# Optimization experiments

Measured on AMD Instinct MI355X. Metric: run time of the kernel, lower is better.

## Reference

```python
import jax, jax.numpy as jnp
import numpy as np

EMB = 512
HEADS = 8
KEY_DIM = 64


def setup_inputs() -> dict:
    key = jax.random.key(0)
    k1, k2, k3, k4, k5 = jax.random.split(key, 5)
    B, S = 4, 2048
    x = jax.random.normal(k1, (B, S, EMB), dtype=jnp.float32)
    keys = jax.random.normal(k2, (B, HEADS, S, KEY_DIM), dtype=jnp.float32)
    values = jax.random.normal(k3, (B, HEADS, S, KEY_DIM), dtype=jnp.float32)
    # torch.rand -> uniform [0,1)
    query_weights = jax.random.uniform(k4, (EMB, KEY_DIM * HEADS), dtype=jnp.float32)
    output_weights = jax.random.uniform(k5, (KEY_DIM * HEADS, EMB), dtype=jnp.float32)
    return {"x": x, "keys": keys, "values": values,
            "query_weights": query_weights, "output_weights": output_weights}


def reference(x, keys, values, query_weights, output_weights):
    B, S, _ = x.shape
    # Q projection: [B,S,E] @ [E,H*K] -> [B,H,S,K]
    q = (x @ query_weights).reshape(B, S, HEADS, KEY_DIM).transpose(0, 2, 1, 3)
    # scores: [B,H,S,S]
    scores = jnp.einsum('bhqk,bhsk->bhqs', q, keys) / jnp.sqrt(jnp.float32(KEY_DIM))
    attn = jax.nn.softmax(scores, axis=-1)
    # context: [B,H,S,K] -> [B,S,H*K]
    ctx = jnp.einsum('bhqs,bhsk->bhqk', attn, values)
    ctx = ctx.transpose(0, 2, 1, 3).reshape(B, S, HEADS * KEY_DIM)
    return ctx @ output_weights
```

## Files before the change

kernel.cpp:

```cpp
#include <hip/hip_runtime.h>
#include <hip/hip_bf16.h>

#define EMB 512
#define HEADS 8
#define KD 64
#define SEQ 2048
#define BATCH 4

typedef __attribute__((ext_vector_type(8))) short bf16x8;
typedef __attribute__((ext_vector_type(4))) float f32x4;

__device__ __forceinline__ unsigned short f2bf(float x) {
    union { float f; unsigned u; } v; v.f = x;
    unsigned r = v.u + 0x7fff + ((v.u >> 16) & 1);
    return (unsigned short)(r >> 16);
}
__device__ __forceinline__ float bf2f(unsigned short b) {
    union { unsigned u; float f; } v; v.u = ((unsigned)b) << 16;
    return v.f;
}

__global__ __launch_bounds__(256) void prep_k_kernel(const float* __restrict__ K,
                                                     unsigned short* __restrict__ kimg) {
    const int bt = blockIdx.x;
    const float4* src = (const float4*)(K + (size_t)bt * 4096);
    unsigned short* dhi = kimg + (size_t)bt * 8192;
    unsigned short* dlo = dhi + 4096;
#pragma unroll
    for (int it = 0; it < 4; ++it) {
        const int idx = threadIdx.x + it * 256;
        const float4 v = src[idx];
        const unsigned short h0 = f2bf(v.x), h1 = f2bf(v.y),
                             h2 = f2bf(v.z), h3 = f2bf(v.w);
        *(uint2*)&dhi[idx * 4] = make_uint2(
            (unsigned)h0 | ((unsigned)h1 << 16),
            (unsigned)h2 | ((unsigned)h3 << 16));
        *(uint2*)&dlo[idx * 4] = make_uint2(
            (unsigned)f2bf(v.x - bf2f(h0)) | ((unsigned)f2bf(v.y - bf2f(h1)) << 16),
            (unsigned)f2bf(v.z - bf2f(h2)) | ((unsigned)f2bf(v.w - bf2f(h3)) << 16));
    }
}

__global__ __launch_bounds__(256) void prep_v_kernel(const float* __restrict__ V,
                                                     unsigned short* __restrict__ vimg) {
    const int bt = blockIdx.x;
    const float* src = V + (size_t)bt * 4096;
    unsigned short* dst = vimg + (size_t)bt * 4096;
#pragma unroll
    for (int it = 0; it < 2; ++it) {
        const int idx = threadIdx.x + it * 256;
        const int sp  = idx & 31;
        const int d4  = (idx >> 5) << 2;
        const float4 a = *(const float4*)(src + (2 * sp) * KD + d4);
        const float4 b = *(const float4*)(src + (2 * sp + 1) * KD + d4);
#pragma unroll
        for (int j = 0; j < 4; ++j) {
            const float aj = (&a.x)[j], bj = (&b.x)[j];
            *(unsigned*)&dst[(d4 + j) * 64 + 2 * sp] =
                (unsigned)f2bf(aj) | ((unsigned)f2bf(bj) << 16);
        }
    }
}

template <int PREP>
__global__ __launch_bounds__(256) void attn3_kernel(const float* __restrict__ Q,
                                                    const float* __restrict__ Keys,
                                                    const float* __restrict__ Vals,
                                                    const unsigned short* __restrict__ kimg,
                                                    const unsigned short* __restrict__ vimg,
                                                    float* __restrict__ out) {
    constexpr int NT  = 64;
    constexpr int LDK = 72;

    __shared__ unsigned short k_s[2][NT][LDK];
    __shared__ unsigned short v_t[KD][LDK];
    __shared__ unsigned short p_s[4][16][LDK];

    const int t  = threadIdx.x;
    const int w  = t >> 6;
    const int l  = t & 63;
    const int g  = l >> 4;
    const int ln = l & 15;

    const int bh = blockIdx.y;
    const int q0 = blockIdx.x * 64 + w * 16;

    const float* kbase = Keys + (size_t)bh * SEQ * KD;
    const float* vbase = Vals + (size_t)bh * SEQ * KD;
    const float* qptr  = Q + ((size_t)bh * SEQ + q0 + ln) * KD;

    bf16x8 qhi[2], qlo[2];
#pragma unroll
    for (int kk = 0; kk < 2; ++kk) {
        const float* p = qptr + g * 8 + 32 * kk;
#pragma unroll
        for (int j = 0; j < 8; ++j) {
            const float x = p[j] * 0.125f;
            const unsigned short h = f2bf(x);
            qhi[kk][j] = (short)h;
            qlo[kk][j] = (short)f2bf(x - bf2f(h));
        }
    }

    f32x4 acc[4];
#pragma unroll
    for (int db = 0; db < 4; ++db) acc[db] = (f32x4){0.f, 0.f, 0.f, 0.f};
    float m_run = -1e30f, l_run = 0.0f;

    for (int tile = 0; tile < SEQ / NT; ++tile) {
        __syncthreads();

        if (PREP) {
            const uint4* ksrc = (const uint4*)(kimg + (size_t)(bh * 32 + tile) * 8192);
#pragma unroll
            for (int it = 0; it < 4; ++it) {
                const int idx = t + it * 256;
                const int hl  = idx >> 9;
                const int rem = idx & 511;
                *(uint4*)&k_s[hl][rem >> 3][(rem & 7) * 8] = ksrc[idx];
            }
            const uint4* vsrc = (const uint4*)(vimg + (size_t)(bh * 32 + tile) * 4096);
#pragma unroll
            for (int it = 0; it < 2; ++it) {
                const int idx = t + it * 256;
                *(uint4*)&v_t[idx >> 3][(idx & 7) * 8] = vsrc[idx];
            }
        } else {
            const float* kt = kbase + (size_t)tile * NT * KD;
            const float* vt = vbase + (size_t)tile * NT * KD;
#pragma unroll
            for (int it = 0; it < 4; ++it) {
                const int idx = t + it * 256;
                const int s   = idx >> 4;
                const int d4  = (idx & 15) << 2;
                const float4 kv = *(const float4*)(kt + s * KD + d4);
                unsigned short h0 = f2bf(kv.x), h1 = f2bf(kv.y),
                               h2 = f2bf(kv.z), h3 = f2bf(kv.w);
                *(uint2*)&k_s[0][s][d4] = make_uint2(
                    (unsigned)h0 | ((unsigned)h1 << 16),
                    (unsigned)h2 | ((unsigned)h3 << 16));
                *(uint2*)&k_s[1][s][d4] = make_uint2(
                    (unsigned)f2bf(kv.x - bf2f(h0)) | ((unsigned)f2bf(kv.y - bf2f(h1)) << 16),
                    (unsigned)f2bf(kv.z - bf2f(h2)) | ((unsigned)f2bf(kv.w - bf2f(h3)) << 16));
            }
#pragma unroll
            for (int it = 0; it < 2; ++it) {
                const int idx = t + it * 256;
                const int sp  = idx & 31;
                const int d4  = (idx >> 5) << 2;
                const float* v0 = vt + (2 * sp) * KD + d4;
                const float4 a = *(const float4*)v0;
                const float4 b = *(const float4*)(v0 + KD);
#pragma unroll
                for (int j = 0; j < 4; ++j) {
                    const float aj = (&a.x)[j], bj = (&b.x)[j];
                    *(unsigned*)&v_t[d4 + j][2 * sp] =
                        (unsigned)f2bf(aj) | ((unsigned)f2bf(bj) << 16);
                }
            }
        }
        __syncthreads();

        f32x4 st[4];
#pragma unroll
        for (int sb = 0; sb < 4; ++sb) {
            f32x4 c = (f32x4){0.f, 0.f, 0.f, 0.f};
#pragma unroll
            for (int kk = 0; kk < 2; ++kk) {
                const bf16x8 khi = *(const bf16x8*)&k_s[0][sb * 16 + ln][g * 8 + 32 * kk];
                const bf16x8 klo = *(const bf16x8*)&k_s[1][sb * 16 + ln][g * 8 + 32 * kk];
                c = __builtin_amdgcn_mfma_f32_16x16x32_bf16(klo, qhi[kk], c, 0, 0, 0);
                c = __builtin_amdgcn_mfma_f32_16x16x32_bf16(khi, qlo[kk], c, 0, 0, 0);
                c = __builtin_amdgcn_mfma_f32_16x16x32_bf16(khi, qhi[kk], c, 0, 0, 0);
            }
            st[sb] = c;
        }

        float tm = st[0][0];
#pragma unroll
        for (int sb = 0; sb < 4; ++sb)
#pragma unroll
            for (int r = 0; r < 4; ++r) tm = fmaxf(tm, st[sb][r]);
        tm = fmaxf(tm, __shfl_xor(tm, 16));
        tm = fmaxf(tm, __shfl_xor(tm, 32));

        const float m_new  = fmaxf(m_run, tm);
        const float scalef = __expf(m_run - m_new);
        m_run = m_new;

        float rs = 0.f;
#pragma unroll
        for (int sb = 0; sb < 4; ++sb) {
            const float p0 = __expf(st[sb][0] - m_new);
            const float p1 = __expf(st[sb][1] - m_new);
            const float p2 = __expf(st[sb][2] - m_new);
            const float p3 = __expf(st[sb][3] - m_new);
            rs += (p0 + p1) + (p2 + p3);
            const unsigned lo = (unsigned)f2bf(p0) | ((unsigned)f2bf(p1) << 16);
            const unsigned hi = (unsigned)f2bf(p2) | ((unsigned)f2bf(p3) << 16);
            *(uint2*)&p_s[w][ln][sb * 16 + g * 4] = make_uint2(lo, hi);
        }
        rs += __shfl_xor(rs, 16);
        rs += __shfl_xor(rs, 32);
        l_run = l_run * scalef + rs;

#pragma unroll
        for (int r = 0; r < 4; ++r) {
            const float sr = __shfl(scalef, 4 * g + r);
#pragma unroll
            for (int db = 0; db < 4; ++db) acc[db][r] *= sr;
        }

        bf16x8 pa[2];
#pragma unroll
        for (int kk = 0; kk < 2; ++kk)
            pa[kk] = *(const bf16x8*)&p_s[w][ln][g * 8 + 32 * kk];
#pragma unroll
        for (int db = 0; db < 4; ++db) {
            f32x4 c = acc[db];
#pragma unroll
            for (int kk = 0; kk < 2; ++kk) {
                const bf16x8 vb = *(const bf16x8*)&v_t[ln + 16 * db][g * 8 + 32 * kk];
                c = __builtin_amdgcn_mfma_f32_16x16x32_bf16(pa[kk], vb, c, 0, 0, 0);
            }
            acc[db] = c;
        }
    }

    const float invl = 1.0f / l_run;
    const int b = bh >> 3, h = bh & 7;
#pragma unroll
    for (int r = 0; r < 4; ++r) {
        const float iv = __shfl(invl, 4 * g + r);
        float* orow = out + ((size_t)(b * SEQ + q0 + 4 * g + r) * EMB) + h * KD + ln;
#pragma unroll
        for (int db = 0; db < 4; ++db) orow[16 * db] = acc[db][r] * iv;
    }
}

template <int TRANSQ>
__global__ __launch_bounds__(256) void proj_mfma_kernel(const float* __restrict__ in,
                                                        const float* __restrict__ W,
                                                        float* __restrict__ out) {
    __shared__ unsigned short x_s[2][64][72];
    __shared__ unsigned short w_t[2][64][72];

    const int t  = threadIdx.x;
    const int w  = t >> 6;
    const int l  = t & 63;
    const int g  = l >> 4;
    const int ln = l & 15;

    const int row0 = blockIdx.x * 64;
    const int n0   = blockIdx.y * 64;

    f32x4 acc[4];
#pragma unroll
    for (int cb = 0; cb < 4; ++cb) acc[cb] = (f32x4){0.f, 0.f, 0.f, 0.f};

    for (int ch = 0; ch < EMB / 64; ++ch) {
        __syncthreads();
#pragma unroll
        for (int it = 0; it < 4; ++it) {
            const int idx = t + it * 256;
            const int s   = idx >> 4;
            const int d4  = (idx & 15) << 2;
            const float4 xv = *(const float4*)(in + (size_t)(row0 + s) * EMB + ch * 64 + d4);
            const unsigned short h0 = f2bf(xv.x), h1 = f2bf(xv.y),
                                 h2 = f2bf(xv.z), h3 = f2bf(xv.w);
            *(uint2*)&x_s[0][s][d4] = make_uint2(
                (unsigned)h0 | ((unsigned)h1 << 16),
                (unsigned)h2 | ((unsigned)h3 << 16));
            *(uint2*)&x_s[1][s][d4] = make_uint2(
                (unsigned)f2bf(xv.x - bf2f(h0)) | ((unsigned)f2bf(xv.y - bf2f(h1)) << 16),
                (unsigned)f2bf(xv.z - bf2f(h2)) | ((unsigned)f2bf(xv.w - bf2f(h3)) << 16));
        }
#pragma unroll
        for (int it = 0; it < 2; ++it) {
            const int idx = t + it * 256;
            const int sp  = idx & 31;
            const int c4  = (idx >> 5) << 2;
            const float* wrow = W + (size_t)(ch * 64 + 2 * sp) * EMB + n0 + c4;
            const float4 a = *(const float4*)wrow;
            const float4 b = *(const float4*)(wrow + EMB);
#pragma unroll
            for (int j = 0; j < 4; ++j) {
                const float aj = (&a.x)[j], bj = (&b.x)[j];
                const unsigned short ah = f2bf(aj), bh = f2bf(bj);
                *(unsigned*)&w_t[0][c4 + j][2 * sp] =
                    (unsigned)ah | ((unsigned)bh << 16);
                *(unsigned*)&w_t[1][c4 + j][2 * sp] =
                    (unsigned)f2bf(aj - bf2f(ah)) | ((unsigned)f2bf(bj - bf2f(bh)) << 16);
            }
        }
        __syncthreads();

        bf16x8 ah[2], al[2];
#pragma unroll
        for (int kk = 0; kk < 2; ++kk) {
            ah[kk] = *(const bf16x8*)&x_s[0][w * 16 + ln][g * 8 + 32 * kk];
            al[kk] = *(const bf16x8*)&x_s[1][w * 16 + ln][g * 8 + 32 * kk];
        }
#pragma unroll
        for (int cb = 0; cb < 4; ++cb) {
            f32x4 c = acc[cb];
#pragma unroll
            for (int kk = 0; kk < 2; ++kk) {
                const bf16x8 bh = *(const bf16x8*)&w_t[0][cb * 16 + ln][g * 8 + 32 * kk];
                const bf16x8 bl = *(const bf16x8*)&w_t[1][cb * 16 + ln][g * 8 + 32 * kk];
                c = __builtin_amdgcn_mfma_f32_16x16x32_bf16(al[kk], bh, c, 0, 0, 0);
                c = __builtin_amdgcn_mfma_f32_16x16x32_bf16(ah[kk], bl, c, 0, 0, 0);
                c = __builtin_amdgcn_mfma_f32_16x16x32_bf16(ah[kk], bh, c, 0, 0, 0);
            }
            acc[cb] = c;
        }
    }

#pragma unroll
    for (int cb = 0; cb < 4; ++cb) {
#pragma unroll
        for (int r = 0; r < 4; ++r) {
            const int row = row0 + w * 16 + 4 * g + r;
            const int col = n0 + cb * 16 + ln;
            if (TRANSQ) {
                const int b = row >> 11, s = row & 2047;
                const int h = col >> 6, k = col & 63;
                out[((size_t)(b * HEADS + h) * SEQ + s) * KD + k] = acc[cb][r];
            } else {
                out[(size_t)row * EMB + col] = acc[cb][r];
            }
        }
    }
}

__global__ __launch_bounds__(256) void proj_fp32_kernel(const float* __restrict__ in,
                                                        const float* __restrict__ W,
                                                        float* __restrict__ out) {
    __shared__ float x_s[8][EMB];
    const int block_row = blockIdx.x * 8;

    const float4* in4 = (const float4*)(in + (size_t)block_row * EMB);
    float4* xs4 = (float4*)(&x_s[0][0]);
    for (int i = threadIdx.x; i < 8 * EMB / 4; i += 256) xs4[i] = in4[i];
    __syncthreads();

    const int n  = (threadIdx.x & 127) * 4;
    const int rg = threadIdx.x >> 7;

    float acc[4][4] = {};
    for (int e = 0; e < EMB; ++e) {
        const float4 w4 = *(const float4*)(W + (size_t)e * EMB + n);
#pragma unroll
        for (int rr = 0; rr < 4; ++rr) {
            const float xv = x_s[rg + rr * 2][e];
            acc[rr][0] += xv * w4.x;
            acc[rr][1] += xv * w4.y;
            acc[rr][2] += xv * w4.z;
            acc[rr][3] += xv * w4.w;
        }
    }
#pragma unroll
    for (int rr = 0; rr < 4; ++rr) {
        const int row = block_row + rg + rr * 2;
        float4 o;
        o.x = acc[rr][0]; o.y = acc[rr][1]; o.z = acc[rr][2]; o.w = acc[rr][3];
        *(float4*)(out + (size_t)row * EMB + n) = o;
    }
}

extern "C" void kernel_launch(void* const* d_in, const int* in_sizes, int n_in,
                              void* d_out, int out_size, void* d_ws, size_t ws_size,
                              hipStream_t stream) {
    const float* x  = (const float*)d_in[0];
    const float* ks = (const float*)d_in[1];
    const float* vs = (const float*)d_in[2];
    const float* wq = (const float*)d_in[3];
    const float* wo = (const float*)d_in[4];
    float* out = (float*)d_out;

    const size_t QBYTES  = (size_t)BATCH * HEADS * SEQ * KD * 4;
    const size_t CBYTES  = (size_t)BATCH * SEQ * EMB * 4;
    const size_t KIBYTES = (size_t)BATCH * HEADS * SEQ * KD * 2 * 2;
    const size_t VIBYTES = (size_t)BATCH * HEADS * SEQ * KD * 2;

    float* Q = (float*)d_ws;
    const bool mid_ws  = ws_size >= QBYTES + CBYTES;
    const bool full_ws = ws_size >= QBYTES + CBYTES + KIBYTES + VIBYTES;
    float* ctx = mid_ws ? (float*)((char*)d_ws + QBYTES) : out;
    unsigned short* kimg = (unsigned short*)((char*)d_ws + QBYTES + CBYTES);
    unsigned short* vimg = (unsigned short*)((char*)d_ws + QBYTES + CBYTES + KIBYTES);

    const int M = BATCH * SEQ;

    proj_mfma_kernel<1><<<dim3(M / 64, EMB / 64), dim3(256), 0, stream>>>(x, wq, Q);

    if (full_ws) {
        prep_k_kernel<<<dim3(BATCH * HEADS * 32), dim3(256), 0, stream>>>(ks, kimg);
        prep_v_kernel<<<dim3(BATCH * HEADS * 32), dim3(256), 0, stream>>>(vs, vimg);
        attn3_kernel<1><<<dim3(SEQ / 64, BATCH * HEADS), dim3(256), 0, stream>>>(
            Q, ks, vs, kimg, vimg, ctx);
    } else {
        attn3_kernel<0><<<dim3(SEQ / 64, BATCH * HEADS), dim3(256), 0, stream>>>(
            Q, ks, vs, nullptr, nullptr, ctx);
    }

    if (mid_ws) {
        proj_mfma_kernel<0><<<dim3(M / 64, EMB / 64), dim3(256), 0, stream>>>(ctx, wo, out);
    } else {
        proj_fp32_kernel<<<dim3(M / 8), dim3(256), 0, stream>>>(ctx, wo, out);
    }
}
```

Measured before the change: 282.3 us.

## Pre-convert all operands to bf16 tile images and chain bf16 kernels

```diff
diff --git a/kernel.cpp b/kernel.cpp
--- a/kernel.cpp
+++ b/kernel.cpp
@@ -18,6 +18,371 @@
 __device__ __forceinline__ float bf2f(unsigned short b) {
     union { unsigned u; float f; } v; v.u = ((unsigned)b) << 16;
     return v.f;
+}
+__device__ __forceinline__ unsigned pk2(float a, float b) {
+    __hip_bfloat162 h = __float22bfloat162_rn(float2{a, b});
+    unsigned u; __builtin_memcpy(&u, &h, 4); return u;
+}
+
+__global__ __launch_bounds__(256) void prep_all_kernel(
+    const float* __restrict__ x,  const float* __restrict__ wq,
+    const float* __restrict__ wo, const float* __restrict__ K,
+    const float* __restrict__ V,
+    unsigned short* __restrict__ ximg, unsigned short* __restrict__ wqimg,
+    unsigned short* __restrict__ woimg, unsigned short* __restrict__ kimg,
+    unsigned short* __restrict__ vimg) {
+    const int bid = blockIdx.x;
+    const int t   = threadIdx.x;
+
+    if (bid < 1024) {
+        const int rb = bid >> 3, ch = bid & 7;
+        const float* src = x + (size_t)rb * 64 * EMB + ch * 64;
+        unsigned short* dhi = ximg + (size_t)bid * 8192;
+        unsigned short* dlo = dhi + 4096;
+#pragma unroll
+        for (int it = 0; it < 4; ++it) {
+            const int idx = t + it * 256;
+            const int row = idx >> 4, c4 = (idx & 15) << 2;
+            const float4 v = *(const float4*)(src + (size_t)row * EMB + c4);
+            const unsigned short h0 = f2bf(v.x), h1 = f2bf(v.y),
+                                 h2 = f2bf(v.z), h3 = f2bf(v.w);
+            *(uint2*)&dhi[row * 64 + c4] = make_uint2(
+                (unsigned)h0 | ((unsigned)h1 << 16),
+                (unsigned)h2 | ((unsigned)h3 << 16));
+            *(uint2*)&dlo[row * 64 + c4] = make_uint2(
+                (unsigned)f2bf(v.x - bf2f(h0)) | ((unsigned)f2bf(v.y - bf2f(h1)) << 16),
+                (unsigned)f2bf(v.z - bf2f(h2)) | ((unsigned)f2bf(v.w - bf2f(h3)) << 16));
+        }
+    } else if (bid < 1152) {
+        int widx = bid - 1024;
+        const bool isq = widx < 64;
+        if (!isq) widx -= 64;
+        const int nb = widx >> 3, ch = widx & 7;
+        const float* src = (isq ? wq : wo) + (size_t)(ch * 64) * EMB + nb * 64;
+        unsigned short* dhi = isq ? (wqimg + (size_t)widx * 8192)
+                                  : (woimg + (size_t)widx * 4096);
+        unsigned short* dlo = dhi + 4096;
+#pragma unroll
+        for (int it = 0; it < 2; ++it) {
+            const int idx = t + it * 256;
+            const int sp  = idx & 31;
+            const int c4  = (idx >> 5) << 2;
+            const float* r0 = src + (size_t)(2 * sp) * EMB + c4;
+            const float4 a = *(const float4*)r0;
+            const float4 b = *(const float4*)(r0 + EMB);
+#pragma unroll
+            for (int j = 0; j < 4; ++j) {
+                const float aj = (&a.x)[j], bj = (&b.x)[j];
+                const unsigned short ah = f2bf(aj), bh = f2bf(bj);
+                *(unsigned*)&dhi[(c4 + j) * 64 + 2 * sp] =
+                    (unsigned)ah | ((unsigned)bh << 16);
+                if (isq)
+                    *(unsigned*)&dlo[(c4 + j) * 64 + 2 * sp] =
+                        (unsigned)f2bf(aj - bf2f(ah)) | ((unsigned)f2bf(bj - bf2f(bh)) << 16);
+            }
+        }
+    } else if (bid < 2176) {
+        const int kt = bid - 1152;
+        const float4* src = (const float4*)(K + (size_t)kt * 4096);
+        unsigned short* dhi = kimg + (size_t)kt * 8192;
+        unsigned short* dlo = dhi + 4096;
+#pragma unroll
+        for (int it = 0; it < 4; ++it) {
+            const int idx = t + it * 256;
+            const float4 v = src[idx];
+            const unsigned short h0 = f2bf(v.x), h1 = f2bf(v.y),
+                                 h2 = f2bf(v.z), h3 = f2bf(v.w);
+            *(uint2*)&dhi[idx * 4] = make_uint2(
+                (unsigned)h0 | ((unsigned)h1 << 16),
+                (unsigned)h2 | ((unsigned)h3 << 16));
+            *(uint2*)&dlo[idx * 4] = make_uint2(
+                (unsigned)f2bf(v.x - bf2f(h0)) | ((unsigned)f2bf(v.y - bf2f(h1)) << 16),
+                (unsigned)f2bf(v.z - bf2f(h2)) | ((unsigned)f2bf(v.w - bf2f(h3)) << 16));
+        }
+    } else {
+        const int vt = bid - 2176;
+        const float* src = V + (size_t)vt * 4096;
+        unsigned short* dst = vimg + (size_t)vt * 4096;
+#pragma unroll
+        for (int it = 0; it < 2; ++it) {
+            const int idx = t + it * 256;
+            const int sp  = idx & 31;
+            const int d4  = (idx >> 5) << 2;
+            const float4 a = *(const float4*)(src + (2 * sp) * KD + d4);
+            const float4 b = *(const float4*)(src + (2 * sp + 1) * KD + d4);
+#pragma unroll
+            for (int j = 0; j < 4; ++j) {
+                *(unsigned*)&dst[(d4 + j) * 64 + 2 * sp] =
+                    (unsigned)f2bf((&a.x)[j]) | ((unsigned)f2bf((&b.x)[j]) << 16);
+            }
+        }
+    }
+}
+
+__global__ __launch_bounds__(256) void proj_q_kernel(
+    const unsigned short* __restrict__ ximg,
+    const unsigned short* __restrict__ wqimg,
+    unsigned short* __restrict__ qhi_img,
+    unsigned short* __restrict__ qlo_img) {
+    __shared__ unsigned short x_s[2][64][72];
+    __shared__ unsigned short w_t[2][64][72];
+
+    const int t  = threadIdx.x;
+    const int w  = t >> 6;
+    const int l  = t & 63;
+    const int g  = l >> 4;
+    const int ln = l & 15;
+
+    const int rb = blockIdx.x;
+    const int nb = blockIdx.y;
+
+    f32x4 acc[4];
+#pragma unroll
+    for (int cb = 0; cb < 4; ++cb) acc[cb] = (f32x4){0.f, 0.f, 0.f, 0.f};
+
+    for (int ch = 0; ch < 8; ++ch) {
+        __syncthreads();
+        const uint4* xs = (const uint4*)(ximg + (size_t)(rb * 8 + ch) * 8192);
+        const uint4* ws = (const uint4*)(wqimg + (size_t)(nb * 8 + ch) * 8192);
+#pragma unroll
+        for (int it = 0; it < 4; ++it) {
+            const int idx = t + it * 256;
+            const int hl  = idx >> 9;
+            const int rem = idx & 511;
+            *(uint4*)&x_s[hl][rem >> 3][(rem & 7) * 8] = xs[idx];
+            *(uint4*)&w_t[hl][rem >> 3][(rem & 7) * 8] = ws[idx];
+        }
+        __syncthreads();
+
+        bf16x8 ah[2], al[2];
+#pragma unroll
+        for (int kk = 0; kk < 2; ++kk) {
+            ah[kk] = *(const bf16x8*)&x_s[0][w * 16 + ln][g * 8 + 32 * kk];
+            al[kk] = *(const bf16x8*)&x_s[1][w * 16 + ln][g * 8 + 32 * kk];
+        }
+#pragma unroll
+        for (int cb = 0; cb < 4; ++cb) {
+            f32x4 c = acc[cb];
+#pragma unroll
+            for (int kk = 0; kk < 2; ++kk) {
+                const bf16x8 bh = *(const bf16x8*)&w_t[0][cb * 16 + ln][g * 8 + 32 * kk];
+                const bf16x8 bl = *(const bf16x8*)&w_t[1][cb * 16 + ln][g * 8 + 32 * kk];
+                c = __builtin_amdgcn_mfma_f32_16x16x32_bf16(al[kk], bh, c, 0, 0, 0);
+                c = __builtin_amdgcn_mfma_f32_16x16x32_bf16(ah[kk], bl, c, 0, 0, 0);
+                c = __builtin_amdgcn_mfma_f32_16x16x32_bf16(ah[kk], bh, c, 0, 0, 0);
+            }
+            acc[cb] = c;
+        }
+    }
+
+#pragma unroll
+    for (int cb = 0; cb < 4; ++cb) {
+#pragma unroll
+        for (int r = 0; r < 4; ++r) {
+            const int row = rb * 64 + w * 16 + 4 * g + r;
+            const int k   = cb * 16 + ln;
+            const float v = acc[cb][r] * 0.125f;
+            const unsigned short hi = f2bf(v);
+            const unsigned short lo = f2bf(v - bf2f(hi));
+            const size_t off = ((size_t)((row >> 11) * HEADS + nb) * SEQ + (row & 2047)) * KD + k;
+            qhi_img[off] = hi;
+            qlo_img[off] = lo;
+        }
+    }
+}
+
+__global__ __launch_bounds__(256) void proj_o_kernel(
+    const unsigned short* __restrict__ ctximg,
+    const unsigned short* __restrict__ woimg,
+    float* __restrict__ out) {
+    __shared__ unsigned short x_s[64][72];
+    __shared__ unsigned short w_t[64][72];
+
+    const int t  = threadIdx.x;
+    const int w  = t >> 6;
+    const int l  = t & 63;
+    const int g  = l >> 4;
+    const int ln = l & 15;
+
+    const int rb = blockIdx.x;
+    const int nb = blockIdx.y;
+
+    f32x4 acc[4];
+#pragma unroll
+    for (int cb = 0; cb < 4; ++cb) acc[cb] = (f32x4){0.f, 0.f, 0.f, 0.f};
+
+    for (int ch = 0; ch < 8; ++ch) {
+        __syncthreads();
+        const uint4* xs = (const uint4*)(ctximg + (size_t)(rb * 8 + ch) * 4096);
+        const uint4* ws = (const uint4*)(woimg + (size_t)(nb * 8 + ch) * 4096);
+#pragma unroll
+        for (int it = 0; it < 2; ++it) {
+            const int idx = t + it * 256;
+            *(uint4*)&x_s[idx >> 3][(idx & 7) * 8] = xs[idx];
+            *(uint4*)&w_t[idx >> 3][(idx & 7) * 8] = ws[idx];
+        }
+        __syncthreads();
+
+        bf16x8 ah[2];
+#pragma unroll
+        for (int kk = 0; kk < 2; ++kk)
+            ah[kk] = *(const bf16x8*)&x_s[w * 16 + ln][g * 8 + 32 * kk];
+#pragma unroll
+        for (int cb = 0; cb < 4; ++cb) {
+            f32x4 c = acc[cb];
+#pragma unroll
+            for (int kk = 0; kk < 2; ++kk) {
+                const bf16x8 bh = *(const bf16x8*)&w_t[cb * 16 + ln][g * 8 + 32 * kk];
+                c = __builtin_amdgcn_mfma_f32_16x16x32_bf16(ah[kk], bh, c, 0, 0, 0);
+            }
+            acc[cb] = c;
+        }
+    }
+
+#pragma unroll
+    for (int cb = 0; cb < 4; ++cb) {
+#pragma unroll
+        for (int r = 0; r < 4; ++r) {
+            const int row = rb * 64 + w * 16 + 4 * g + r;
+            const int col = nb * 64 + cb * 16 + ln;
+            out[(size_t)row * EMB + col] = acc[cb][r];
+        }
+    }
+}
+
+__global__ __launch_bounds__(256) void attn4_kernel(
+    const unsigned short* __restrict__ qhi_img,
+    const unsigned short* __restrict__ qlo_img,
+    const unsigned short* __restrict__ kimg,
+    const unsigned short* __restrict__ vimg,
+    unsigned short* __restrict__ ctximg) {
+    constexpr int NT  = 64;
+    constexpr int LDK = 72;
+
+    __shared__ unsigned short k_s[2][NT][LDK];
+    __shared__ unsigned short v_t[KD][LDK];
+    __shared__ unsigned short p_s[4][16][LDK];
+
+    const int t  = threadIdx.x;
+    const int w  = t >> 6;
+    const int l  = t & 63;
+    const int g  = l >> 4;
+    const int ln = l & 15;
+
+    const int bh = blockIdx.y;
+    const int q0 = blockIdx.x * 64 + w * 16;
+
+    bf16x8 qhi[2], qlo[2];
+    {
+        const size_t qoff = ((size_t)bh * SEQ + q0 + ln) * KD;
+#pragma unroll
+        for (int kk = 0; kk < 2; ++kk) {
+            qhi[kk] = *(const bf16x8*)&qhi_img[qoff + g * 8 + 32 * kk];
+            qlo[kk] = *(const bf16x8*)&qlo_img[qoff + g * 8 + 32 * kk];
+        }
+    }
+
+    f32x4 acc[4];
+#pragma unroll
+    for (int db = 0; db < 4; ++db) acc[db] = (f32x4){0.f, 0.f, 0.f, 0.f};
+    float m_run = -1e30f, l_run = 0.0f;
+
+    for (int tile = 0; tile < SEQ / NT; ++tile) {
+        __syncthreads();
+
+        const uint4* ksrc = (const uint4*)(kimg + (size_t)(bh * 32 + tile) * 8192);
+#pragma unroll
+        for (int it = 0; it < 4; ++it) {
+            const int idx = t + it * 256;
+            const int hl  = idx >> 9;
+            const int rem = idx & 511;
+            *(uint4*)&k_s[hl][rem >> 3][(rem & 7) * 8] = ksrc[idx];
+        }
+        const uint4* vsrc = (const uint4*)(vimg + (size_t)(bh * 32 + tile) * 4096);
+#pragma unroll
+        for (int it = 0; it < 2; ++it) {
+            const int idx = t + it * 256;
+            *(uint4*)&v_t[idx >> 3][(idx & 7) * 8] = vsrc[idx];
+        }
+        __syncthreads();
+
+        f32x4 st[4];
+#pragma unroll
+        for (int sb = 0; sb < 4; ++sb) {
+            f32x4 c = (f32x4){0.f, 0.f, 0.f, 0.f};
+#pragma unroll
+            for (int kk = 0; kk < 2; ++kk) {
+                const bf16x8 khi = *(const bf16x8*)&k_s[0][sb * 16 + ln][g * 8 + 32 * kk];
+                const bf16x8 klo = *(const bf16x8*)&k_s[1][sb * 16 + ln][g * 8 + 32 * kk];
+                c = __builtin_amdgcn_mfma_f32_16x16x32_bf16(klo, qhi[kk], c, 0, 0, 0);
+                c = __builtin_amdgcn_mfma_f32_16x16x32_bf16(khi, qlo[kk], c, 0, 0, 0);
+                c = __builtin_amdgcn_mfma_f32_16x16x32_bf16(khi, qhi[kk], c, 0, 0, 0);
+            }
+            st[sb] = c;
+        }
+
+        float tm = st[0][0];
+#pragma unroll
+        for (int sb = 0; sb < 4; ++sb)
+#pragma unroll
+            for (int r = 0; r < 4; ++r) tm = fmaxf(tm, st[sb][r]);
+        tm = fmaxf(tm, __shfl_xor(tm, 16));
+        tm = fmaxf(tm, __shfl_xor(tm, 32));
+
+        const float m_new  = fmaxf(m_run, tm);
+        const float scalef = __expf(m_run - m_new);
+        m_run = m_new;
+
+        float rs = 0.f;
+#pragma unroll
+        for (int sb = 0; sb < 4; ++sb) {
+            const float p0 = __expf(st[sb][0] - m_new);
+            const float p1 = __expf(st[sb][1] - m_new);
+            const float p2 = __expf(st[sb][2] - m_new);
+            const float p3 = __expf(st[sb][3] - m_new);
+            rs += (p0 + p1) + (p2 + p3);
+            *(uint2*)&p_s[w][ln][sb * 16 + g * 4] =
+                make_uint2(pk2(p0, p1), pk2(p2, p3));
+        }
+        rs += __shfl_xor(rs, 16);
+        rs += __shfl_xor(rs, 32);
+        l_run = l_run * scalef + rs;
+
+#pragma unroll
+        for (int r = 0; r < 4; ++r) {
+            const float sr = __shfl(scalef, 4 * g + r);
+#pragma unroll
+            for (int db = 0; db < 4; ++db) acc[db][r] *= sr;
+        }
+
+        bf16x8 pa[2];
+#pragma unroll
+        for (int kk = 0; kk < 2; ++kk)
+            pa[kk] = *(const bf16x8*)&p_s[w][ln][g * 8 + 32 * kk];
+#pragma unroll
+        for (int db = 0; db < 4; ++db) {
+            f32x4 c = acc[db];
+#pragma unroll
+            for (int kk = 0; kk < 2; ++kk) {
+                const bf16x8 vb = *(const bf16x8*)&v_t[ln + 16 * db][g * 8 + 32 * kk];
+                c = __builtin_amdgcn_mfma_f32_16x16x32_bf16(pa[kk], vb, c, 0, 0, 0);
+            }
+            acc[db] = c;
+        }
+    }
+
+    const float invl = 1.0f / l_run;
+    const int rb  = (bh >> 3) * 32 + blockIdx.x;
+    const int chh = bh & 7;
+    unsigned short* cbase = ctximg + ((size_t)rb * 8 + chh) * 4096;
+#pragma unroll
+    for (int r = 0; r < 4; ++r) {
+        const float iv = __shfl(invl, 4 * g + r);
+        const int row = w * 16 + 4 * g + r;
+#pragma unroll
+        for (int db = 0; db < 4; ++db)
+            cbase[row * 64 + db * 16 + ln] = f2bf(acc[db][r] * iv);
+    }
 }
 
 __global__ __launch_bounds__(256) void prep_k_kernel(const float* __restrict__ K,
@@ -55,9 +420,8 @@
         const float4 b = *(const float4*)(src + (2 * sp + 1) * KD + d4);
 #pragma unroll
         for (int j = 0; j < 4; ++j) {
-            const float aj = (&a.x)[j], bj = (&b.x)[j];
             *(unsigned*)&dst[(d4 + j) * 64 + 2 * sp] =
-                (unsigned)f2bf(aj) | ((unsigned)f2bf(bj) << 16);
+                (unsigned)f2bf((&a.x)[j]) | ((unsigned)f2bf((&b.x)[j]) << 16);
         }
     }
 }
@@ -95,10 +459,10 @@
         const float* p = qptr + g * 8 + 32 * kk;
 #pragma unroll
         for (int j = 0; j < 8; ++j) {
-            const float x = p[j] * 0.125f;
-            const unsigned short h = f2bf(x);
+            const float xv = p[j] * 0.125f;
+            const unsigned short h = f2bf(xv);
             qhi[kk][j] = (short)h;
-            qlo[kk][j] = (short)f2bf(x - bf2f(h));
+            qlo[kk][j] = (short)f2bf(xv - bf2f(h));
         }
     }
 
@@ -153,9 +517,8 @@
                 const float4 b = *(const float4*)(v0 + KD);
 #pragma unroll
                 for (int j = 0; j < 4; ++j) {
-                    const float aj = (&a.x)[j], bj = (&b.x)[j];
                     *(unsigned*)&v_t[d4 + j][2 * sp] =
-                        (unsigned)f2bf(aj) | ((unsigned)f2bf(bj) << 16);
+                        (unsigned)f2bf((&a.x)[j]) | ((unsigned)f2bf((&b.x)[j]) << 16);
                 }
             }
         }
@@ -196,9 +559,8 @@
             const float p2 = __expf(st[sb][2] - m_new);
             const float p3 = __expf(st[sb][3] - m_new);
             rs += (p0 + p1) + (p2 + p3);
-            const unsigned lo = (unsigned)f2bf(p0) | ((unsigned)f2bf(p1) << 16);
-            const unsigned hi = (unsigned)f2bf(p2) | ((unsigned)f2bf(p3) << 16);
-            *(uint2*)&p_s[w][ln][sb * 16 + g * 4] = make_uint2(lo, hi);
+            *(uint2*)&p_s[w][ln][sb * 16 + g * 4] =
+                make_uint2(pk2(p0, p1), pk2(p2, p3));
         }
         rs += __shfl_xor(rs, 16);
         rs += __shfl_xor(rs, 32);
@@ -378,6 +740,37 @@
     const float* wo = (const float*)d_in[4];
     float* out = (float*)d_out;
 
+    const int M = BATCH * SEQ;
+
+    const size_t XIMG_OFF = 0;
+    const size_t WQ_OFF   = 16777216;
+    const size_t WO_OFF   = 17825792;
+    const size_t KIMG_OFF = 18350080;
+    const size_t VIMG_OFF = 35127296;
+    const size_t QHI_OFF  = 43515904;
+    const size_t QLO_OFF  = 51904512;
+    const size_t CTX_OFF  = 60293120;
+    const size_t TIER_A   = 68681728;
+
+    if (ws_size >= TIER_A) {
+        unsigned short* ximg  = (unsigned short*)((char*)d_ws + XIMG_OFF);
+        unsigned short* wqimg = (unsigned short*)((char*)d_ws + WQ_OFF);
+        unsigned short* woimg = (unsigned short*)((char*)d_ws + WO_OFF);
+        unsigned short* kimg  = (unsigned short*)((char*)d_ws + KIMG_OFF);
+        unsigned short* vimg  = (unsigned short*)((char*)d_ws + VIMG_OFF);
+        unsigned short* qhi   = (unsigned short*)((char*)d_ws + QHI_OFF);
+        unsigned short* qlo   = (unsigned short*)((char*)d_ws + QLO_OFF);
+        unsigned short* ctx   = (unsigned short*)((char*)d_ws + CTX_OFF);
+
+        prep_all_kernel<<<dim3(3200), dim3(256), 0, stream>>>(
+            x, wq, wo, ks, vs, ximg, wqimg, woimg, kimg, vimg);
+        proj_q_kernel<<<dim3(M / 64, HEADS), dim3(256), 0, stream>>>(ximg, wqimg, qhi, qlo);
+        attn4_kernel<<<dim3(SEQ / 64, BATCH * HEADS), dim3(256), 0, stream>>>(
+            qhi, qlo, kimg, vimg, ctx);
+        proj_o_kernel<<<dim3(M / 64, EMB / 64), dim3(256), 0, stream>>>(ctx, woimg, out);
+        return;
+    }
+
     const size_t QBYTES  = (size_t)BATCH * HEADS * SEQ * KD * 4;
     const size_t CBYTES  = (size_t)BATCH * SEQ * EMB * 4;
     const size_t KIBYTES = (size_t)BATCH * HEADS * SEQ * KD * 2 * 2;
@@ -386,11 +779,9 @@
     float* Q = (float*)d_ws;
     const bool mid_ws  = ws_size >= QBYTES + CBYTES;
     const bool full_ws = ws_size >= QBYTES + CBYTES + KIBYTES + VIBYTES;
-    float* ctx = mid_ws ? (float*)((char*)d_ws + QBYTES) : out;
+    float* ctxf = mid_ws ? (float*)((char*)d_ws + QBYTES) : out;
     unsigned short* kimg = (unsigned short*)((char*)d_ws + QBYTES + CBYTES);
     unsigned short* vimg = (unsigned short*)((char*)d_ws + QBYTES + CBYTES + KIBYTES);
-
-    const int M = BATCH * SEQ;
 
     proj_mfma_kernel<1><<<dim3(M / 64, EMB / 64), dim3(256), 0, stream>>>(x, wq, Q);
 
@@ -398,15 +789,15 @@
         prep_k_kernel<<<dim3(BATCH * HEADS * 32), dim3(256), 0, stream>>>(ks, kimg);
         prep_v_kernel<<<dim3(BATCH * HEADS * 32), dim3(256), 0, stream>>>(vs, vimg);
         attn3_kernel<1><<<dim3(SEQ / 64, BATCH * HEADS), dim3(256), 0, stream>>>(
-            Q, ks, vs, kimg, vimg, ctx);
+            Q, ks, vs, kimg, vimg, ctxf);
     } else {
         attn3_kernel<0><<<dim3(SEQ / 64, BATCH * HEADS), dim3(256), 0, stream>>>(
-            Q, ks, vs, nullptr, nullptr, ctx);
+            Q, ks, vs, nullptr, nullptr, ctxf);
     }
 
     if (mid_ws) {
-        proj_mfma_kernel<0><<<dim3(M / 64, EMB / 64), dim3(256), 0, stream>>>(ctx, wo, out);
+        proj_mfma_kernel<0><<<dim3(M / 64, EMB / 64), dim3(256), 0, stream>>>(ctxf, wo, out);
     } else {
-        proj_fp32_kernel<<<dim3(M / 8), dim3(256), 0, stream>>>(ctx, wo, out);
-    }
-}
+        proj_fp32_kernel<<<dim3(M / 8), dim3(256), 0, stream>>>(ctxf, wo, out);
+    }
+}
```

Result: faster. 245.3 us (-13.1%).
